# Performance work log

Hardware: AMD Instinct MI355X
Metric: run time of the kernel (lower is better)

Reference implementation:

```python
import jax, jax.numpy as jnp
import numpy as np

N_NODES = 50000
N_EDGES = 800000
IN_FEATS = 128
OUT_FEATS = 128


def setup_inputs() -> dict:
    key = jax.random.key(0)
    k_feat, k_src, k_dst, k_w1, k_w2, k_lw = jax.random.split(key, 6)
    feat = jax.random.normal(k_feat, (N_NODES, IN_FEATS), dtype=jnp.float32)
    src_idx = jax.random.randint(k_src, (N_EDGES,), 0, N_NODES, dtype=jnp.int64 if jax.config.jax_enable_x64 else jnp.int32)
    dst_idx = jax.random.randint(k_dst, (N_EDGES,), 0, N_NODES, dtype=jnp.int64 if jax.config.jax_enable_x64 else jnp.int32)
    # xavier-uniform-ish scales
    w1_lim = float(np.sqrt(6.0 / (2 * IN_FEATS + IN_FEATS)))
    w2_lim = float(np.sqrt(6.0 / (IN_FEATS + OUT_FEATS)))
    lw_lim = float(np.sqrt(2.0) * np.sqrt(6.0 / (IN_FEATS + OUT_FEATS)))
    weight1 = jax.random.uniform(k_w1, (2 * IN_FEATS, IN_FEATS), jnp.float32, -w1_lim, w1_lim)
    weight2 = jax.random.uniform(k_w2, (IN_FEATS, OUT_FEATS), jnp.float32, -w2_lim, w2_lim)
    loop_weight = jax.random.uniform(k_lw, (IN_FEATS, OUT_FEATS), jnp.float32, -lw_lim, lw_lim)
    bias = jnp.zeros((OUT_FEATS,), dtype=jnp.float32)
    return {
        "feat": feat,
        "src_idx": src_idx,
        "dst_idx": dst_idx,
        "weight1": weight1,
        "weight2": weight2,
        "loop_weight": loop_weight,
        "bias": bias,
    }


def reference(feat, src_idx, dst_idx, weight1, weight2, loop_weight, bias):
    # Gather per-edge src/dst features and concat: [E, 2*d]
    feat_msg = jnp.concatenate([feat[src_idx], feat[dst_idx]], axis=-1)
    # 2-layer edge MLP: relu(msg @ W1) @ W2 -> [E, out]
    e_msg = jnp.matmul(jax.nn.relu(jnp.matmul(feat_msg, weight1)), weight2)
    # Scatter-sum to destination nodes: [N, out]
    rst = jax.ops.segment_sum(e_msg, dst_idx, num_segments=feat.shape[0])
    # bias + residual loop message
    rst = rst + bias + jnp.matmul(feat, loop_weight)
    return rst
```

## Files before the change

### kernel.cpp

```cpp
#include <hip/hip_runtime.h>

typedef __attribute__((ext_vector_type(8))) unsigned short ushort8v;
typedef __attribute__((ext_vector_type(8))) short short8v;
typedef __attribute__((ext_vector_type(4))) float f32x4;

__device__ inline unsigned short f2bf(float f) {
    union { float f; unsigned u; } v; v.f = f;
    unsigned u = v.u;
    unsigned r = (u + 0x7FFFu + ((u >> 16) & 1u)) >> 16;
    return (unsigned short)r;
}
__device__ inline float bf2f(unsigned short h) {
    union { unsigned u; float f; } v; v.u = ((unsigned)h) << 16;
    return v.f;
}

#define CAP 64

__global__ __launch_bounds__(256) void fused_pre(
    const float* __restrict__ feat, unsigned short* __restrict__ X2, int totalF,
    const float* __restrict__ W1, const float* __restrict__ W2,
    const float* __restrict__ LW,
    unsigned short* __restrict__ W1t, unsigned short* __restrict__ W3t,
    int cvtB) {
    int b = blockIdx.x, t = threadIdx.x;
    if (b < cvtB) {
        int idx = (b * 256 + t) * 4;
        if (idx >= totalF) return;
        float4 v = *(const float4*)(feat + idx);
        int row = idx >> 7, col = idx & 127;
        unsigned short* o = X2 + (size_t)row * 256 + 128 + col;
        *(ushort4*)o = make_ushort4(f2bf(v.x), f2bf(v.y), f2bf(v.z), f2bf(v.w));
    } else {
        int i = (b - cvtB) * 256 + t;
        if (i < 32768) {
            int jj = i >> 7, k = i & 127;
            float v = (jj < 128) ? W1[k * 128 + jj] : W1[(128 + k) * 128 + (jj - 128)];
            W1t[i] = f2bf(v);
        } else {
            int i2 = i - 32768;
            int n = i2 >> 8, k = i2 & 255;
            float v = (k < 128) ? W2[k * 128 + n] : LW[(k - 128) * 128 + n];
            W3t[i2] = f2bf(v);
        }
    }
}

template <bool OUT_BF16>
__device__ void gemm_tile(
    unsigned short* As, unsigned short* Bs,
    const unsigned short* __restrict__ A, int lda,
    const unsigned short* __restrict__ Bt, int ldb, int nRowsB,
    void* __restrict__ Cout, int ldc,
    const float* __restrict__ bias, int M, int K, int m0, int n0) {
    const int tid = threadIdx.x;
    const int lane = tid & 63;
    const int w = tid >> 6;
    const int wr = w >> 1, wc = w & 1;
    const int q = lane >> 4, ln = lane & 15;

    f32x4 acc[4][4];
#pragma unroll
    for (int i = 0; i < 4; i++)
#pragma unroll
        for (int j = 0; j < 4; j++) acc[i][j] = (f32x4)0.f;

    for (int kk = 0; kk < K; kk += 64) {
#pragma unroll
        for (int i = 0; i < 4; i++) {
            int id = i * 256 + tid;
            int r = id >> 3, b = id & 7;
            ushort8v v = (ushort8v)(unsigned short)0;
            int gr = m0 + r;
            if (gr < M) v = *(const ushort8v*)(A + (size_t)gr * lda + kk + b * 8);
            *(ushort8v*)(As + r * 64 + ((b ^ (r & 7)) * 8)) = v;
        }
#pragma unroll
        for (int i = 0; i < 4; i++) {
            int id = i * 256 + tid;
            int r = id >> 3, b = id & 7;
            ushort8v v = (ushort8v)(unsigned short)0;
            int gr = n0 + r;
            if (gr < nRowsB) v = *(const ushort8v*)(Bt + (size_t)gr * ldb + kk + b * 8);
            *(ushort8v*)(Bs + r * 64 + ((b ^ (r & 7)) * 8)) = v;
        }
        __syncthreads();
#pragma unroll
        for (int ks = 0; ks < 2; ks++) {
            short8v af[4], bfv[4];
#pragma unroll
            for (int ti = 0; ti < 4; ti++) {
                int m = wr * 64 + ti * 16 + ln;
                int blk = (ks * 4 + q) ^ (m & 7);
                af[ti] = *(const short8v*)(As + m * 64 + blk * 8);
            }
#pragma unroll
            for (int tj = 0; tj < 4; tj++) {
                int n = wc * 64 + tj * 16 + ln;
                int blk = (ks * 4 + q) ^ (n & 7);
                bfv[tj] = *(const short8v*)(Bs + n * 64 + blk * 8);
            }
#pragma unroll
            for (int ti = 0; ti < 4; ti++)
#pragma unroll
                for (int tj = 0; tj < 4; tj++)
                    acc[ti][tj] = __builtin_amdgcn_mfma_f32_16x16x32_bf16(
                        af[ti], bfv[tj], acc[ti][tj], 0, 0, 0);
        }
        __syncthreads();
    }

#pragma unroll
    for (int ti = 0; ti < 4; ti++) {
        int rowb = m0 + wr * 64 + ti * 16 + q * 4;
#pragma unroll
        for (int tj = 0; tj < 4; tj++) {
            int col = n0 + wc * 64 + tj * 16 + ln;
            f32x4 c = acc[ti][tj];
            float bv = 0.f;
            if (!OUT_BF16 && bias) bv = bias[col];
#pragma unroll
            for (int r = 0; r < 4; r++) {
                int row = rowb + r;
                if (row < M) {
                    if (OUT_BF16)
                        ((unsigned short*)Cout)[(size_t)row * ldc + col] = f2bf(c[r]);
                    else
                        ((float*)Cout)[(size_t)row * ldc + col] = c[r] + bv;
                }
            }
        }
    }
}

__global__ __launch_bounds__(256) void gemm1_scatter(
    const unsigned short* __restrict__ X2feat, const unsigned short* __restrict__ W1t,
    unsigned short* __restrict__ AB,
    const int* __restrict__ src, const int* __restrict__ dst,
    int* __restrict__ cur, unsigned short* __restrict__ eSrc,
    int E, int gemmB, int N) {
    __shared__ unsigned short smem[2 * 128 * 64];
    int b = blockIdx.x;
    int half = b >> 1;
    if ((b & 1) == 0) {
        if (half >= gemmB) return;
        int m0 = (half >> 1) * 128, n0 = (half & 1) * 128;
        gemm_tile<true>(smem, smem + 128 * 64, X2feat, 256, W1t, 128, 256,
                        (void*)AB, 256, nullptr, N, 128, m0, n0);
    } else {
        int e = (half * 256 + threadIdx.x) * 4;
        if (e + 3 < E) {
            int4 s4 = *(const int4*)(src + e);
            int4 d4 = *(const int4*)(dst + e);
            int p0 = atomicAdd(&cur[d4.x], 1);
            int p1 = atomicAdd(&cur[d4.y], 1);
            int p2 = atomicAdd(&cur[d4.z], 1);
            int p3 = atomicAdd(&cur[d4.w], 1);
            eSrc[(size_t)d4.x * CAP + min(p0, CAP - 1)] = (unsigned short)s4.x;
            eSrc[(size_t)d4.y * CAP + min(p1, CAP - 1)] = (unsigned short)s4.y;
            eSrc[(size_t)d4.z * CAP + min(p2, CAP - 1)] = (unsigned short)s4.z;
            eSrc[(size_t)d4.w * CAP + min(p3, CAP - 1)] = (unsigned short)s4.w;
        } else {
            for (int i = e; i < E && i >= 0; i++) {
                int d = dst[i];
                int pos = atomicAdd(&cur[d], 1);
                eSrc[(size_t)d * CAP + min(pos, CAP - 1)] = (unsigned short)src[i];
            }
        }
    }
}

__global__ __launch_bounds__(256) void gather_kernel(
    const unsigned short* __restrict__ AB, const int* __restrict__ cur,
    const unsigned short* __restrict__ eSrc,
    unsigned short* __restrict__ X2, int N) {
    int wid = (blockIdx.x * 256 + threadIdx.x) >> 6;
    int lane = threadIdx.x & 63;
    if (wid >= N) return;
    int num = min(cur[wid], CAP);
    size_t start = (size_t)wid * CAP;
    int half = lane >> 5, ln32 = lane & 31;
    ushort4 bv = *(const ushort4*)(AB + (size_t)wid * 256 + 128 + ln32 * 4);
    float b0 = bf2f(bv.x), b1 = bf2f(bv.y), b2 = bf2f(bv.z), b3 = bf2f(bv.w);
    float p0 = 0.f, p1 = 0.f, p2 = 0.f, p3 = 0.f;

    int mySrc = (lane < num) ? (int)eSrc[start + lane] : 0;
    int j = 0;
    for (; j + 8 <= num; j += 8) {
        ushort4 v[4];
#pragma unroll
        for (int u = 0; u < 4; u++) {
            int s = __shfl(mySrc, j + 2 * u + half);
            v[u] = *(const ushort4*)(AB + (size_t)s * 256 + ln32 * 4);
        }
#pragma unroll
        for (int u = 0; u < 4; u++) {
            p0 += fmaxf(bf2f(v[u].x) + b0, 0.f);
            p1 += fmaxf(bf2f(v[u].y) + b1, 0.f);
            p2 += fmaxf(bf2f(v[u].z) + b2, 0.f);
            p3 += fmaxf(bf2f(v[u].w) + b3, 0.f);
        }
    }
    for (; j < num; j += 2) {
        int idx = j + half;
        int s = __shfl(mySrc, idx);
        bool ok = idx < num;
        ushort4 v = *(const ushort4*)(AB + (size_t)s * 256 + ln32 * 4);
        float m = ok ? 1.f : 0.f;
        p0 += m * fmaxf(bf2f(v.x) + b0, 0.f);
        p1 += m * fmaxf(bf2f(v.y) + b1, 0.f);
        p2 += m * fmaxf(bf2f(v.z) + b2, 0.f);
        p3 += m * fmaxf(bf2f(v.w) + b3, 0.f);
    }
    p0 += __shfl_xor(p0, 32);
    p1 += __shfl_xor(p1, 32);
    p2 += __shfl_xor(p2, 32);
    p3 += __shfl_xor(p3, 32);
    if (half == 0) {
        *(ushort4*)(X2 + (size_t)wid * 256 + ln32 * 4) =
            make_ushort4(f2bf(p0), f2bf(p1), f2bf(p2), f2bf(p3));
    }
}

template <bool OUT_BF16>
__global__ __launch_bounds__(256) void gemm128(
    const unsigned short* __restrict__ A, int lda,
    const unsigned short* __restrict__ Bt, int ldb, int nRowsB,
    void* __restrict__ Cout, int ldc,
    const float* __restrict__ bias, int M, int K) {
    __shared__ unsigned short smem[2 * 128 * 64];
    gemm_tile<OUT_BF16>(smem, smem + 128 * 64, A, lda, Bt, ldb, nRowsB,
                        Cout, ldc, bias, M, K, blockIdx.x * 128, blockIdx.y * 128);
}

extern "C" void kernel_launch(void* const* d_in, const int* in_sizes, int n_in,
                              void* d_out, int out_size, void* d_ws, size_t ws_size,
                              hipStream_t stream) {
    const float* feat = (const float*)d_in[0];
    const int* src = (const int*)d_in[1];
    const int* dst = (const int*)d_in[2];
    const float* W1 = (const float*)d_in[3];
    const float* W2 = (const float*)d_in[4];
    const float* LW = (const float*)d_in[5];
    const float* bias = (const float*)d_in[6];
    float* out = (float*)d_out;

    const int N = in_sizes[0] / 128;
    const int E = in_sizes[1];

    char* ws = (char*)d_ws;
    unsigned short* X2 = (unsigned short*)ws;
    size_t off_b = (size_t)N * 256 * 2;
    unsigned short* AB = (unsigned short*)(ws + off_b);
    off_b += (size_t)N * 256 * 2;
    unsigned short* W1t = (unsigned short*)(ws + off_b);
    off_b += (size_t)256 * 128 * 2;
    unsigned short* W3t = (unsigned short*)(ws + off_b);
    off_b += (size_t)128 * 256 * 2;
    int* cur = (int*)(ws + off_b);             off_b += (size_t)N * 4;
    unsigned short* eSrc = (unsigned short*)(ws + off_b);
    off_b += (size_t)N * CAP * 2;

    int totalF = N * 128;
    int cvtB = (totalF / 4 + 255) / 256;

    hipMemsetAsync(cur, 0, (size_t)N * 4, stream);
    fused_pre<<<cvtB + 256, 256, 0, stream>>>(
        feat, X2, totalF, W1, W2, LW, W1t, W3t, cvtB);

    int gemmB = ((N + 127) / 128) * 2;
    int scatB = ((E + 3) / 4 + 255) / 256;
    int mx = gemmB > scatB ? gemmB : scatB;
    gemm1_scatter<<<2 * mx, 256, 0, stream>>>(
        X2 + 128, W1t, AB, src, dst, cur, eSrc, E, gemmB, N);

    gather_kernel<<<(N + 3) / 4, 256, 0, stream>>>(AB, cur, eSrc, X2, N);

    dim3 g2((N + 127) / 128, 1);
    gemm128<false><<<g2, 256, 0, stream>>>(X2, 256, W3t, 256, 128,
                                           (void*)out, 128, bias, N, 256);
}
```

Measured before the change: 182.8 us.

## Fuse neighbor gather with second GEMM using LDS-resident aggregated tile

Replaces the separate gather kernel and final GEMM with one kernel. Each block aggregates 128 destination rows into a swizzled LDS tile and feeds it directly into MFMA together with the loop-feature half. This removes the global write and reread of the aggregated features and one launch. The cost is far fewer blocks doing the latency-bound gather, which reduces parallelism. Source indices are also widened from 16-bit to 32-bit, doubling that buffer's traffic.

```diff
diff --git a/kernel.cpp b/kernel.cpp
--- a/kernel.cpp
+++ b/kernel.cpp
@@ -46,13 +46,12 @@
     }
 }
 
-template <bool OUT_BF16>
-__device__ void gemm_tile(
+__device__ void gemm_tile_bf16out(
     unsigned short* As, unsigned short* Bs,
     const unsigned short* __restrict__ A, int lda,
     const unsigned short* __restrict__ Bt, int ldb, int nRowsB,
-    void* __restrict__ Cout, int ldc,
-    const float* __restrict__ bias, int M, int K, int m0, int n0) {
+    unsigned short* __restrict__ Cout, int ldc,
+    int M, int K, int m0, int n0) {
     const int tid = threadIdx.x;
     const int lane = tid & 63;
     const int w = tid >> 6;
@@ -117,17 +116,10 @@
         for (int tj = 0; tj < 4; tj++) {
             int col = n0 + wc * 64 + tj * 16 + ln;
             f32x4 c = acc[ti][tj];
-            float bv = 0.f;
-            if (!OUT_BF16 && bias) bv = bias[col];
 #pragma unroll
             for (int r = 0; r < 4; r++) {
                 int row = rowb + r;
-                if (row < M) {
-                    if (OUT_BF16)
-                        ((unsigned short*)Cout)[(size_t)row * ldc + col] = f2bf(c[r]);
-                    else
-                        ((float*)Cout)[(size_t)row * ldc + col] = c[r] + bv;
-                }
+                if (row < M) Cout[(size_t)row * ldc + col] = f2bf(c[r]);
             }
         }
     }
@@ -137,7 +129,7 @@
     const unsigned short* __restrict__ X2feat, const unsigned short* __restrict__ W1t,
     unsigned short* __restrict__ AB,
     const int* __restrict__ src, const int* __restrict__ dst,
-    int* __restrict__ cur, unsigned short* __restrict__ eSrc,
+    int* __restrict__ cur, int* __restrict__ eSrc,
     int E, int gemmB, int N) {
     __shared__ unsigned short smem[2 * 128 * 64];
     int b = blockIdx.x;
@@ -145,8 +137,8 @@
     if ((b & 1) == 0) {
         if (half >= gemmB) return;
         int m0 = (half >> 1) * 128, n0 = (half & 1) * 128;
-        gemm_tile<true>(smem, smem + 128 * 64, X2feat, 256, W1t, 128, 256,
-                        (void*)AB, 256, nullptr, N, 128, m0, n0);
+        gemm_tile_bf16out(smem, smem + 128 * 64, X2feat, 256, W1t, 128, 256,
+                          AB, 256, N, 128, m0, n0);
     } else {
         int e = (half * 256 + threadIdx.x) * 4;
         if (e + 3 < E) {
@@ -156,81 +148,159 @@
             int p1 = atomicAdd(&cur[d4.y], 1);
             int p2 = atomicAdd(&cur[d4.z], 1);
             int p3 = atomicAdd(&cur[d4.w], 1);
-            eSrc[(size_t)d4.x * CAP + min(p0, CAP - 1)] = (unsigned short)s4.x;
-            eSrc[(size_t)d4.y * CAP + min(p1, CAP - 1)] = (unsigned short)s4.y;
-            eSrc[(size_t)d4.z * CAP + min(p2, CAP - 1)] = (unsigned short)s4.z;
-            eSrc[(size_t)d4.w * CAP + min(p3, CAP - 1)] = (unsigned short)s4.w;
+            eSrc[(size_t)d4.x * CAP + min(p0, CAP - 1)] = s4.x;
+            eSrc[(size_t)d4.y * CAP + min(p1, CAP - 1)] = s4.y;
+            eSrc[(size_t)d4.z * CAP + min(p2, CAP - 1)] = s4.z;
+            eSrc[(size_t)d4.w * CAP + min(p3, CAP - 1)] = s4.w;
         } else {
             for (int i = e; i < E && i >= 0; i++) {
                 int d = dst[i];
                 int pos = atomicAdd(&cur[d], 1);
-                eSrc[(size_t)d * CAP + min(pos, CAP - 1)] = (unsigned short)src[i];
-            }
-        }
-    }
-}
-
-__global__ __launch_bounds__(256) void gather_kernel(
+                eSrc[(size_t)d * CAP + min(pos, CAP - 1)] = src[i];
+            }
+        }
+    }
+}
+
+__global__ __launch_bounds__(256) void gather_gemm2(
     const unsigned short* __restrict__ AB, const int* __restrict__ cur,
-    const unsigned short* __restrict__ eSrc,
-    unsigned short* __restrict__ X2, int N) {
-    int wid = (blockIdx.x * 256 + threadIdx.x) >> 6;
-    int lane = threadIdx.x & 63;
-    if (wid >= N) return;
-    int num = min(cur[wid], CAP);
-    size_t start = (size_t)wid * CAP;
-    int half = lane >> 5, ln32 = lane & 31;
-    ushort4 bv = *(const ushort4*)(AB + (size_t)wid * 256 + 128 + ln32 * 4);
-    float b0 = bf2f(bv.x), b1 = bf2f(bv.y), b2 = bf2f(bv.z), b3 = bf2f(bv.w);
-    float p0 = 0.f, p1 = 0.f, p2 = 0.f, p3 = 0.f;
-
-    int mySrc = (lane < num) ? (int)eSrc[start + lane] : 0;
-    int j = 0;
-    for (; j + 8 <= num; j += 8) {
-        ushort4 v[4];
-#pragma unroll
-        for (int u = 0; u < 4; u++) {
-            int s = __shfl(mySrc, j + 2 * u + half);
-            v[u] = *(const ushort4*)(AB + (size_t)s * 256 + ln32 * 4);
-        }
-#pragma unroll
-        for (int u = 0; u < 4; u++) {
-            p0 += fmaxf(bf2f(v[u].x) + b0, 0.f);
-            p1 += fmaxf(bf2f(v[u].y) + b1, 0.f);
-            p2 += fmaxf(bf2f(v[u].z) + b2, 0.f);
-            p3 += fmaxf(bf2f(v[u].w) + b3, 0.f);
-        }
-    }
-    for (; j < num; j += 2) {
-        int idx = j + half;
-        int s = __shfl(mySrc, idx);
-        bool ok = idx < num;
-        ushort4 v = *(const ushort4*)(AB + (size_t)s * 256 + ln32 * 4);
-        float m = ok ? 1.f : 0.f;
-        p0 += m * fmaxf(bf2f(v.x) + b0, 0.f);
-        p1 += m * fmaxf(bf2f(v.y) + b1, 0.f);
-        p2 += m * fmaxf(bf2f(v.z) + b2, 0.f);
-        p3 += m * fmaxf(bf2f(v.w) + b3, 0.f);
-    }
-    p0 += __shfl_xor(p0, 32);
-    p1 += __shfl_xor(p1, 32);
-    p2 += __shfl_xor(p2, 32);
-    p3 += __shfl_xor(p3, 32);
-    if (half == 0) {
-        *(ushort4*)(X2 + (size_t)wid * 256 + ln32 * 4) =
-            make_ushort4(f2bf(p0), f2bf(p1), f2bf(p2), f2bf(p3));
-    }
-}
-
-template <bool OUT_BF16>
-__global__ __launch_bounds__(256) void gemm128(
-    const unsigned short* __restrict__ A, int lda,
-    const unsigned short* __restrict__ Bt, int ldb, int nRowsB,
-    void* __restrict__ Cout, int ldc,
-    const float* __restrict__ bias, int M, int K) {
-    __shared__ unsigned short smem[2 * 128 * 64];
-    gemm_tile<OUT_BF16>(smem, smem + 128 * 64, A, lda, Bt, ldb, nRowsB,
-                        Cout, ldc, bias, M, K, blockIdx.x * 128, blockIdx.y * 128);
+    const int* __restrict__ eSrc, const unsigned short* __restrict__ X2feat,
+    const unsigned short* __restrict__ W3t, const float* __restrict__ bias,
+    float* __restrict__ out, int N) {
+    __shared__ unsigned short Sg[128 * 128];
+    __shared__ unsigned short Bs[128 * 64];
+    const int tid = threadIdx.x;
+    const int lane = tid & 63;
+    const int w = tid >> 6;
+    const int m0 = blockIdx.x * 128;
+    const int half = lane >> 5, ln32 = lane & 31;
+
+    for (int rr = w; rr < 128; rr += 4) {
+        int row = m0 + rr;
+        int kb = ln32 >> 1;
+        int sgoff = rr * 128 + ((kb ^ (rr & 15)) * 8) + (ln32 & 1) * 4;
+        if (row >= N) {
+            if (half == 0) *(ushort4*)(Sg + sgoff) = make_ushort4(0, 0, 0, 0);
+            continue;
+        }
+        int num = min(cur[row], CAP);
+        size_t start = (size_t)row * CAP;
+        ushort4 bv = *(const ushort4*)(AB + (size_t)row * 256 + 128 + ln32 * 4);
+        float b0 = bf2f(bv.x), b1 = bf2f(bv.y), b2 = bf2f(bv.z), b3 = bf2f(bv.w);
+        float p0 = 0.f, p1 = 0.f, p2 = 0.f, p3 = 0.f;
+        int mySrc = (lane < num) ? eSrc[start + lane] : 0;
+        int j = 0;
+        for (; j + 8 <= num; j += 8) {
+            ushort4 v[4];
+#pragma unroll
+            for (int u = 0; u < 4; u++) {
+                int s = __shfl(mySrc, j + 2 * u + half);
+                v[u] = *(const ushort4*)(AB + (size_t)s * 256 + ln32 * 4);
+            }
+#pragma unroll
+            for (int u = 0; u < 4; u++) {
+                p0 += fmaxf(bf2f(v[u].x) + b0, 0.f);
+                p1 += fmaxf(bf2f(v[u].y) + b1, 0.f);
+                p2 += fmaxf(bf2f(v[u].z) + b2, 0.f);
+                p3 += fmaxf(bf2f(v[u].w) + b3, 0.f);
+            }
+        }
+        for (; j < num; j += 2) {
+            int idx = j + half;
+            int s = __shfl(mySrc, idx);
+            bool ok = idx < num;
+            ushort4 v = *(const ushort4*)(AB + (size_t)s * 256 + ln32 * 4);
+            float m = ok ? 1.f : 0.f;
+            p0 += m * fmaxf(bf2f(v.x) + b0, 0.f);
+            p1 += m * fmaxf(bf2f(v.y) + b1, 0.f);
+            p2 += m * fmaxf(bf2f(v.z) + b2, 0.f);
+            p3 += m * fmaxf(bf2f(v.w) + b3, 0.f);
+        }
+        p0 += __shfl_xor(p0, 32);
+        p1 += __shfl_xor(p1, 32);
+        p2 += __shfl_xor(p2, 32);
+        p3 += __shfl_xor(p3, 32);
+        if (half == 0)
+            *(ushort4*)(Sg + sgoff) = make_ushort4(f2bf(p0), f2bf(p1), f2bf(p2), f2bf(p3));
+    }
+    __syncthreads();
+
+    const int wr = w >> 1, wc = w & 1;
+    const int q = lane >> 4, ln = lane & 15;
+    f32x4 acc[4][4];
+#pragma unroll
+    for (int i = 0; i < 4; i++)
+#pragma unroll
+        for (int j = 0; j < 4; j++) acc[i][j] = (f32x4)0.f;
+
+    unsigned short* As = Sg;
+    for (int kk2 = 0; kk2 < 4; kk2++) {
+        int kk = kk2 * 64;
+        if (kk2 >= 2) {
+#pragma unroll
+            for (int i = 0; i < 4; i++) {
+                int id = i * 256 + tid;
+                int r = id >> 3, b = id & 7;
+                ushort8v v = (ushort8v)(unsigned short)0;
+                int gr = m0 + r;
+                if (gr < N)
+                    v = *(const ushort8v*)(X2feat + (size_t)gr * 256 + (kk - 128) + b * 8);
+                *(ushort8v*)(As + r * 64 + ((b ^ (r & 7)) * 8)) = v;
+            }
+        }
+#pragma unroll
+        for (int i = 0; i < 4; i++) {
+            int id = i * 256 + tid;
+            int r = id >> 3, b = id & 7;
+            ushort8v v = *(const ushort8v*)(W3t + (size_t)r * 256 + kk + b * 8);
+            *(ushort8v*)(Bs + r * 64 + ((b ^ (r & 7)) * 8)) = v;
+        }
+        __syncthreads();
+#pragma unroll
+        for (int ks = 0; ks < 2; ks++) {
+            short8v af[4], bfv[4];
+#pragma unroll
+            for (int ti = 0; ti < 4; ti++) {
+                int m = wr * 64 + ti * 16 + ln;
+                if (kk2 < 2) {
+                    int blk = (kk2 * 8 + ks * 4 + q) ^ (m & 15);
+                    af[ti] = *(const short8v*)(Sg + m * 128 + blk * 8);
+                } else {
+                    int blk = (ks * 4 + q) ^ (m & 7);
+                    af[ti] = *(const short8v*)(As + m * 64 + blk * 8);
+                }
+            }
+#pragma unroll
+            for (int tj = 0; tj < 4; tj++) {
+                int n = wc * 64 + tj * 16 + ln;
+                int blk = (ks * 4 + q) ^ (n & 7);
+                bfv[tj] = *(const short8v*)(Bs + n * 64 + blk * 8);
+            }
+#pragma unroll
+            for (int ti = 0; ti < 4; ti++)
+#pragma unroll
+                for (int tj = 0; tj < 4; tj++)
+                    acc[ti][tj] = __builtin_amdgcn_mfma_f32_16x16x32_bf16(
+                        af[ti], bfv[tj], acc[ti][tj], 0, 0, 0);
+        }
+        __syncthreads();
+    }
+
+#pragma unroll
+    for (int ti = 0; ti < 4; ti++) {
+        int rowb = m0 + wr * 64 + ti * 16 + q * 4;
+#pragma unroll
+        for (int tj = 0; tj < 4; tj++) {
+            int col = wc * 64 + tj * 16 + ln;
+            f32x4 c = acc[ti][tj];
+            float bv = bias[col];
+#pragma unroll
+            for (int r = 0; r < 4; r++) {
+                int row = rowb + r;
+                if (row < N) out[(size_t)row * 128 + col] = c[r] + bv;
+            }
+        }
+    }
 }
 
 extern "C" void kernel_launch(void* const* d_in, const int* in_sizes, int n_in,
@@ -257,9 +327,8 @@
     off_b += (size_t)256 * 128 * 2;
     unsigned short* W3t = (unsigned short*)(ws + off_b);
     off_b += (size_t)128 * 256 * 2;
-    int* cur = (int*)(ws + off_b);             off_b += (size_t)N * 4;
-    unsigned short* eSrc = (unsigned short*)(ws + off_b);
-    off_b += (size_t)N * CAP * 2;
+    int* cur = (int*)(ws + off_b);   off_b += (size_t)N * 4;
+    int* eSrc = (int*)(ws + off_b);  off_b += (size_t)N * CAP * 4;
 
     int totalF = N * 128;
     int cvtB = (totalF / 4 + 255) / 256;
@@ -274,9 +343,6 @@
     gemm1_scatter<<<2 * mx, 256, 0, stream>>>(
         X2 + 128, W1t, AB, src, dst, cur, eSrc, E, gemmB, N);
 
-    gather_kernel<<<(N + 3) / 4, 256, 0, stream>>>(AB, cur, eSrc, X2, N);
-
-    dim3 g2((N + 127) / 128, 1);
-    gemm128<false><<<g2, 256, 0, stream>>>(X2, 256, W3t, 256, 128,
-                                           (void*)out, 128, bias, N, 256);
-}
+    gather_gemm2<<<(N + 127) / 128, 256, 0, stream>>>(
+        AB, cur, eSrc, X2 + 128, W3t, bias, out, N);
+}
```

New measurement: 224.6 us. 22.8% more time.
